# Performance work log

Hardware: AMD Instinct MI355X
Metric: run time of the kernel (lower is better)

## Reference

```python
import jax, jax.numpy as jnp
import numpy as np

D = 1024  # in_features
H = 16    # head_num

def setup_inputs() -> dict:
    key = jax.random.key(0)
    ks = jax.random.split(key, 11)
    S, B = 2048, 2
    scale = 1.0 / np.sqrt(D)
    inp = {
        'q': jax.random.normal(ks[0], (S, B, D), jnp.float32),
        'k': jax.random.normal(ks[1], (S, B, D), jnp.float32),
        'v': jax.random.normal(ks[2], (S, B, D), jnp.float32),
        'Wq': jax.random.normal(ks[3], (D, D), jnp.float32) * scale,
        'Wk': jax.random.normal(ks[4], (D, D), jnp.float32) * scale,
        'Wv': jax.random.normal(ks[5], (D, D), jnp.float32) * scale,
        'Wo': jax.random.normal(ks[6], (D, D), jnp.float32) * scale,
        'bq': jax.random.normal(ks[7], (D,), jnp.float32) * 0.01,
        'bk': jax.random.normal(ks[8], (D,), jnp.float32) * 0.01,
        'bv': jax.random.normal(ks[9], (D,), jnp.float32) * 0.01,
        'bo': jax.random.normal(ks[10], (D,), jnp.float32) * 0.01,
    }
    return inp

def reference(q, k, v, Wq, Wk, Wv, Wo, bq, bk, bv, bo):
    # q,k,v: (S, B, D) -> (B, S, D)
    q = jnp.transpose(q, (1, 0, 2))
    k = jnp.transpose(k, (1, 0, 2))
    v = jnp.transpose(v, (1, 0, 2))
    # linear + ReLU (torch Linear: x @ W.T + b)
    qh = jax.nn.relu(q @ Wq.T + bq)
    kh = jax.nn.relu(k @ Wk.T + bk)
    vh = jax.nn.relu(v @ Wv.T + bv)
    B, S, _ = qh.shape
    hd = D // H
    # (B, S, H, hd) -> (B, H, S, hd)
    qh = qh.reshape(B, S, H, hd).transpose(0, 2, 1, 3)
    kh = kh.reshape(B, S, H, hd).transpose(0, 2, 1, 3)
    vh = vh.reshape(B, S, H, hd).transpose(0, 2, 1, 3)
    scores = jnp.einsum('bhsd,bhtd->bhst', qh, kh) / np.sqrt(hd).astype(np.float32)
    attn = jax.nn.softmax(scores, axis=-1)
    y = jnp.einsum('bhst,bhtd->bhsd', attn, vh)  # (B, H, S, hd)
    y = y.transpose(0, 2, 1, 3).reshape(B, S, D)
    y = jax.nn.relu(y @ Wo.T + bo)
    return jnp.transpose(y, (1, 0, 2))  # (S, B, D)
```

## Files before the change

### kernel.cpp

```cpp
#include <hip/hip_runtime.h>
#include <stdint.h>

typedef __attribute__((ext_vector_type(8))) short bf8v;
typedef __attribute__((ext_vector_type(4))) float f4v;
typedef __attribute__((ext_vector_type(16))) float f16v;
typedef __attribute__((ext_vector_type(4))) unsigned int u4v;

__device__ __forceinline__ unsigned short f2bf(float f) {
  unsigned int u = __float_as_uint(f);
  u += 0x7fffu + ((u >> 16) & 1u);
  return (unsigned short)(u >> 16);
}

__device__ __forceinline__ unsigned short f2h(float f) {
  _Float16 h = (_Float16)f;
  return __builtin_bit_cast(unsigned short, h);
}

__device__ __forceinline__ float h2f(unsigned short s) {
  return (float)__builtin_bit_cast(_Float16, s);
}

__device__ __forceinline__ void gload16(const void* g, void* l) {
  __builtin_amdgcn_global_load_lds(
      (__attribute__((address_space(1))) void*)reinterpret_cast<uintptr_t>(g),
      (__attribute__((address_space(3))) void*)reinterpret_cast<uintptr_t>(l),
      16, 0, 0);
}

__device__ __forceinline__ unsigned cvtpk(float lo, float hi) {
  unsigned r;
  asm("v_cvt_pk_bf16_f32 %0, %1, %2" : "=v"(r) : "v"(lo), "v"(hi));
  return r;
}

#define PAIR_SWAP(x, y) asm("v_permlane32_swap_b32 %0, %1" : "+v"(x), "+v"(y))

__global__ __launch_bounds__(256) void cvt_w(
    const float* __restrict__ s0, const float* __restrict__ s1,
    const float* __restrict__ s2, const float* __restrict__ s3,
    unsigned short* __restrict__ dst) {
  const size_t NW = (size_t)1 << 20;
  size_t i = ((size_t)blockIdx.x * 256 + threadIdx.x) * 8;
  int a = (int)(i >> 20);
  const float* src = (a == 0) ? s0 : (a == 1) ? s1 : (a == 2) ? s2 : s3;
  size_t off = i & (NW - 1);
  const f4v* sp = (const f4v*)(src + off);
  f4v x = sp[0], y = sp[1];
  bf8v r;
  r[0] = (short)f2bf(x[0]); r[1] = (short)f2bf(x[1]);
  r[2] = (short)f2bf(x[2]); r[3] = (short)f2bf(x[3]);
  r[4] = (short)f2bf(y[0]); r[5] = (short)f2bf(y[1]);
  r[6] = (short)f2bf(y[2]); r[7] = (short)f2bf(y[3]);
  *(bf8v*)(dst + i) = r;
}

template <int OMODE>
__device__ __forceinline__ void gemmA32r_body(
    unsigned short* Al, unsigned short* Bl,
    const float* __restrict__ A, const unsigned short* __restrict__ W,
    const float* __restrict__ bias, unsigned short* __restrict__ out) {
  const int tid = threadIdx.x;
  const int w = tid >> 6, l = tid & 63;
  const int lr = l >> 4, lc = l & 15;
  const int m0 = blockIdx.x * 128, n0 = blockIdx.y * 128;
  const int wr = w >> 1, wc = w & 1;

  f4v acc[4][4];
#pragma unroll
  for (int i = 0; i < 4; i++)
#pragma unroll
    for (int j = 0; j < 4; j++) acc[i][j] = (f4v)(0.0f);

  int eA[2], rA[2], kA[2];
#pragma unroll
  for (int i = 0; i < 2; i++) {
    int chunk = w * 2 + i;
    eA[i] = chunk * 512 + l * 8;
    rA[i] = eA[i] >> 5;
    kA[i] = eA[i] & 31;
  }

  const int NK = 32;
  f4v ar[2][2];

  auto A_LOAD = [&](int kk) {
#pragma unroll
    for (int i = 0; i < 2; i++) {
      const float* s = A + (size_t)(m0 + rA[i]) * 1024 + kk * 32 + kA[i];
      ar[i][0] = *(const f4v*)s;
      ar[i][1] = *(const f4v*)(s + 4);
    }
  };
  auto A_WRITE = [&](int buf) {
#pragma unroll
    for (int i = 0; i < 2; i++) {
      u4v aw;
      aw[0] = cvtpk(ar[i][0][0], ar[i][0][1]);
      aw[1] = cvtpk(ar[i][0][2], ar[i][0][3]);
      aw[2] = cvtpk(ar[i][1][0], ar[i][1][1]);
      aw[3] = cvtpk(ar[i][1][2], ar[i][1][3]);
      *(bf8v*)(Al + buf * 4096 + eA[i]) = __builtin_bit_cast(bf8v, aw);
    }
  };
  auto B_STAGE = [&](int buf, int kk) {
#pragma unroll
    for (int i = 0; i < 2; i++) {
      int chunk = w * 2 + i;
      int e = chunk * 512 + l * 8;
      int r = e >> 5, k = e & 31;
      gload16(W + (size_t)(n0 + r) * 1024 + kk * 32 + k, Bl + buf * 4096 + chunk * 512);
    }
  };

  A_LOAD(0);
  B_STAGE(0, 0);
  A_WRITE(0);
  __syncthreads();

  for (int kk = 0; kk < NK; kk++) {
    const int cur = kk & 1;
    const bool more = (kk + 1 < NK);
    if (more) {
      A_LOAD(kk + 1);
      B_STAGE(cur ^ 1, kk + 1);
    }
    bf8v av[4], bv[4];
#pragma unroll
    for (int i = 0; i < 4; i++) {
      int row = wr * 64 + i * 16 + lc;
      av[i] = *(const bf8v*)(Al + cur * 4096 + row * 32 + lr * 8);
    }
#pragma unroll
    for (int j = 0; j < 4; j++) {
      int row = wc * 64 + j * 16 + lc;
      bv[j] = *(const bf8v*)(Bl + cur * 4096 + row * 32 + lr * 8);
    }
#pragma unroll
    for (int i = 0; i < 4; i++)
#pragma unroll
      for (int j = 0; j < 4; j++)
        acc[i][j] = __builtin_amdgcn_mfma_f32_16x16x32_bf16(av[i], bv[j], acc[i][j], 0, 0, 0);
    if (more) A_WRITE(cur ^ 1);
    __syncthreads();
  }

#pragma unroll
  for (int j = 0; j < 4; j++) {
    int n = n0 + wc * 64 + j * 16 + lc;
    float bj = bias[n];
#pragma unroll
    for (int i = 0; i < 4; i++) {
      int mb = m0 + wr * 64 + i * 16 + lr * 4;
#pragma unroll
      for (int q = 0; q < 4; q++) {
        float val = fmaxf(acc[i][j][q] + bj, 0.0f);
        int m = mb + q;
        int s = m >> 1, b = m & 1;
        int h = n >> 6, d = n & 63;
        if (OMODE == 0)
          out[((size_t)(b * 16 + h) * 2048 + s) * 64 + d] = f2bf(val);
        else
          out[((size_t)(b * 16 + h) * 64 + d) * 2048 + s] = f2bf(val);
      }
    }
  }
}

__global__ __launch_bounds__(256) void qkv_gemm(
    const float* __restrict__ qA, const float* __restrict__ kA,
    const float* __restrict__ vA,
    const unsigned short* __restrict__ Wq, const unsigned short* __restrict__ Wk,
    const unsigned short* __restrict__ Wv,
    const float* __restrict__ bq, const float* __restrict__ bk,
    const float* __restrict__ bv,
    unsigned short* __restrict__ Qh, unsigned short* __restrict__ Kh,
    unsigned short* __restrict__ Vt) {
  __shared__ __align__(16) unsigned short Al[2 * 4096];
  __shared__ __align__(16) unsigned short Bl[2 * 4096];
  int z = blockIdx.z;
  if (z == 0)      gemmA32r_body<0>(Al, Bl, qA, Wq, bq, Qh);
  else if (z == 1) gemmA32r_body<0>(Al, Bl, kA, Wk, bk, Kh);
  else             gemmA32r_body<1>(Al, Bl, vA, Wv, bv, Vt);
}

template <int TN>
__device__ __forceinline__ void gemm_body2(
    unsigned short* Al, unsigned short* Bl,
    const unsigned short* __restrict__ A, const unsigned short* __restrict__ W,
    const float* __restrict__ bias, float* __restrict__ out) {
  const int tid = threadIdx.x;
  const int w = tid >> 6, l = tid & 63;
  const int lr = l >> 4, lc = l & 15;
  const int m0 = blockIdx.x * 128, n0 = blockIdx.y * TN;
  const int wr = w >> 1, wc = w & 1;
  const int JW = TN / 32;
  const int BCPW = TN / 64;
  const int BBUF = TN * 32;

  f4v acc[4][JW];
#pragma unroll
  for (int i = 0; i < 4; i++)
#pragma unroll
    for (int j = 0; j < JW; j++) acc[i][j] = (f4v)(0.0f);

  const int NK = 32;
#pragma unroll
  for (int i = 0; i < 2; i++) {
    int chunk = w * 2 + i;
    int e = chunk * 512 + l * 8;
    int r = e >> 5, k = e & 31;
    gload16(A + (size_t)(m0 + r) * 1024 + k, Al + chunk * 512);
  }
#pragma unroll
  for (int i = 0; i < BCPW; i++) {
    int chunk = w * BCPW + i;
    int e = chunk * 512 + l * 8;
    int r = e >> 5, k = e & 31;
    gload16(W + (size_t)(n0 + r) * 1024 + k, Bl + chunk * 512);
  }

  for (int kk = 0; kk < NK; kk++) {
    const int cur = kk & 1;
    __syncthreads();
    if (kk + 1 < NK) {
#pragma unroll
      for (int i = 0; i < 2; i++) {
        int chunk = w * 2 + i;
        int e = chunk * 512 + l * 8;
        int r = e >> 5, k = (kk + 1) * 32 + (e & 31);
        gload16(A + (size_t)(m0 + r) * 1024 + k, Al + (cur ^ 1) * 4096 + chunk * 512);
      }
#pragma unroll
      for (int i = 0; i < BCPW; i++) {
        int chunk = w * BCPW + i;
        int e = chunk * 512 + l * 8;
        int r = e >> 5, k = (kk + 1) * 32 + (e & 31);
        gload16(W + (size_t)(n0 + r) * 1024 + k, Bl + (cur ^ 1) * BBUF + chunk * 512);
      }
    }
    bf8v av[4], bv[JW];
#pragma unroll
    for (int i = 0; i < 4; i++) {
      int row = wr * 64 + i * 16 + lc;
      av[i] = *(const bf8v*)(Al + cur * 4096 + row * 32 + lr * 8);
    }
#pragma unroll
    for (int j = 0; j < JW; j++) {
      int row = wc * (TN / 2) + j * 16 + lc;
      bv[j] = *(const bf8v*)(Bl + cur * BBUF + row * 32 + lr * 8);
    }
#pragma unroll
    for (int i = 0; i < 4; i++)
#pragma unroll
      for (int j = 0; j < JW; j++)
        acc[i][j] = __builtin_amdgcn_mfma_f32_16x16x32_bf16(av[i], bv[j], acc[i][j], 0, 0, 0);
  }

#pragma unroll
  for (int j = 0; j < JW; j++) {
    int n = n0 + wc * (TN / 2) + j * 16 + lc;
    float bj = bias[n];
#pragma unroll
    for (int i = 0; i < 4; i++) {
      int mb = m0 + wr * 64 + i * 16 + lr * 4;
#pragma unroll
      for (int q = 0; q < 4; q++) {
        float val = fmaxf(acc[i][j][q] + bj, 0.0f);
        int m = mb + q;
        int s = m & 2047, b = m >> 11;
        out[(size_t)(s * 2 + b) * 1024 + n] = val;
      }
    }
  }
}

__global__ __launch_bounds__(256) void out_gemm(
    const unsigned short* __restrict__ Y, const unsigned short* __restrict__ Wo,
    const float* __restrict__ bo, float* __restrict__ out) {
  __shared__ __align__(16) unsigned short Al[2 * 4096];
  __shared__ __align__(16) unsigned short Bl[2 * 2048];
  gemm_body2<64>(Al, Bl, Y, Wo, bo, out);
}

__global__ __launch_bounds__(256, 2) void attn_kernel(
    const unsigned short* __restrict__ Qh, const unsigned short* __restrict__ Kh,
    const unsigned short* __restrict__ Vt,
    unsigned short* __restrict__ PO, float2* __restrict__ ML, int kvlen) {
  __shared__ __align__(16) unsigned short Kl[2][4096];
  __shared__ __align__(16) unsigned short Vl[2][4096];
  const int tid = threadIdx.x, w = tid >> 6, l = tid & 63;
  const int lo = l & 31, hi = l >> 5;
  const int bh = blockIdx.y;
  const int z = blockIdx.z;
  const int tbeg = z * kvlen, tend = tbeg + kvlen;
  const int q0 = blockIdx.x * 256 + w * 64;
  const size_t qkbase = (size_t)bh * 2048 * 64;
  const size_t vtbase = (size_t)bh * 64 * 2048;
  const float cs = 0.125f * 1.44269504088896341f;

  bf8v qf[2][4];
#pragma unroll
  for (int s = 0; s < 2; s++)
#pragma unroll
    for (int c = 0; c < 4; c++)
      qf[s][c] = *(const bf8v*)(Qh + qkbase + (size_t)(q0 + s * 32 + lo) * 64 + c * 16 + hi * 8);

  f16v oacc[2][2];
  oacc[0][0] = (f16v)(0.0f); oacc[0][1] = (f16v)(0.0f);
  oacc[1][0] = (f16v)(0.0f); oacc[1][1] = (f16v)(0.0f);
  float mrun[2] = {-1e30f, -1e30f};
  float lrun[2] = {0.0f, 0.0f};

  const int swl = (lo & 7) << 4;
  int akb[4], avb[2][2][2];
#pragma unroll
  for (int c = 0; c < 4; c++) akb[c] = lo * 128 + ((c * 32 + hi * 16) ^ swl);
#pragma unroll
  for (int dt = 0; dt < 2; dt++)
#pragma unroll
    for (int kvh = 0; kvh < 2; kvh++)
#pragma unroll
      for (int kc = 0; kc < 2; kc++)
        avb[dt][kvh][kc] = (dt * 32 + lo) * 128 + ((kvh * 64 + kc * 32 + hi * 16) ^ swl);

  int stE[2], stD[2], stKV[2];
#pragma unroll
  for (int i = 0; i < 2; i++) {
    int o = (w * 2 + i) * 1024 + l * 16;
    int row = o >> 7;
    stE[i] = (o ^ ((row & 7) << 4)) >> 1;
    stD[i] = stE[i] >> 6;
    stKV[i] = stE[i] & 63;
  }
  const char* KlB = (const char*)&Kl[0][0];
  const char* VlB = (const char*)&Vl[0][0];

  auto STAGE = [&](int buf, int t0) {
#pragma unroll
    for (int i = 0; i < 2; i++) {
      gload16(Kh + qkbase + (size_t)t0 * 64 + stE[i], (char*)&Kl[buf][0] + (w * 2 + i) * 1024);
      gload16(Vt + vtbase + (size_t)stD[i] * 2048 + t0 + stKV[i], (char*)&Vl[buf][0] + (w * 2 + i) * 1024);
    }
  };

  auto COMPUTE = [&](int bo) {
#pragma unroll
    for (int kvh = 0; kvh < 2; kvh++) {
      bf8v kf[4];
#pragma unroll
      for (int c = 0; c < 4; c++)
        kf[c] = *(const bf8v*)(KlB + bo + kvh * 4096 + akb[c]);
      f16v sa = (f16v)(0.0f), sb = (f16v)(0.0f);
      __builtin_amdgcn_s_setprio(1);
#pragma unroll
      for (int c = 0; c < 4; c++) {
        sa = __builtin_amdgcn_mfma_f32_32x32x16_bf16(kf[c], qf[0][c], sa, 0, 0, 0);
        sb = __builtin_amdgcn_mfma_f32_32x32x16_bf16(kf[c], qf[1][c], sb, 0, 0, 0);
      }
      __builtin_amdgcn_s_setprio(0);
      bf8v vf[2][2];
#pragma unroll
      for (int dt = 0; dt < 2; dt++)
#pragma unroll
        for (int kc = 0; kc < 2; kc++)
          vf[dt][kc] = *(const bf8v*)(VlB + bo + avb[dt][kvh][kc]);

#pragma unroll
      for (int s = 0; s < 2; s++) {
        const f16v& sc16 = (s == 0) ? sa : sb;
        float t0 = fmaxf(fmaxf(sc16[0], sc16[1]), sc16[2]);
        float t1 = fmaxf(fmaxf(sc16[3], sc16[4]), sc16[5]);
        float t2 = fmaxf(fmaxf(sc16[6], sc16[7]), sc16[8]);
        float t3 = fmaxf(fmaxf(sc16[9], sc16[10]), sc16[11]);
        float t4 = fmaxf(fmaxf(sc16[12], sc16[13]), sc16[14]);
        float lm = fmaxf(fmaxf(fmaxf(t0, t1), fmaxf(t2, t3)), fmaxf(t4, sc16[15]));
        float msc = lm * cs;
        if (!__all(msc <= mrun[s] + 5.0f)) {
          float x = msc, y = msc;
          PAIR_SWAP(x, y);
          float pm = fmaxf(x, y);
          float mnew = fmaxf(mrun[s], pm);
          float scl = __builtin_amdgcn_exp2f(mrun[s] - mnew);
          lrun[s] *= scl;
#pragma unroll
          for (int dt = 0; dt < 2; dt++)
#pragma unroll
            for (int r = 0; r < 16; r++) oacc[s][dt][r] *= scl;
          mrun[s] = mnew;
        }
        float p[16];
#pragma unroll
        for (int r = 0; r < 16; r++)
          p[r] = __builtin_amdgcn_exp2f(sc16[r] * cs - mrun[s]);
        float s01 = (p[0] + p[1]) + (p[2] + p[3]);
        float s23 = (p[4] + p[5]) + (p[6] + p[7]);
        float s45 = (p[8] + p[9]) + (p[10] + p[11]);
        float s67 = (p[12] + p[13]) + (p[14] + p[15]);
        lrun[s] += (s01 + s23) + (s45 + s67);
        bf8v pf[2];
#pragma unroll
        for (int kc = 0; kc < 2; kc++) {
          unsigned a0 = cvtpk(p[kc * 8 + 0], p[kc * 8 + 1]);
          unsigned a1 = cvtpk(p[kc * 8 + 2], p[kc * 8 + 3]);
          unsigned b0 = cvtpk(p[kc * 8 + 4], p[kc * 8 + 5]);
          unsigned b1 = cvtpk(p[kc * 8 + 6], p[kc * 8 + 7]);
          PAIR_SWAP(a0, b0);
          PAIR_SWAP(a1, b1);
          u4v pw;
          pw[0] = a0; pw[1] = a1; pw[2] = b0; pw[3] = b1;
          pf[kc] = __builtin_bit_cast(bf8v, pw);
        }
        __builtin_amdgcn_s_setprio(1);
#pragma unroll
        for (int dt = 0; dt < 2; dt++)
#pragma unroll
          for (int kc = 0; kc < 2; kc++)
            oacc[s][dt] = __builtin_amdgcn_mfma_f32_32x32x16_bf16(vf[dt][kc], pf[kc],
                                                                 oacc[s][dt], 0, 0, 0);
        __builtin_amdgcn_s_setprio(0);
      }
    }
  };

  STAGE(0, tbeg);
  __syncthreads();
#pragma unroll 1
  for (int t0 = tbeg; t0 < tend; t0 += 128) {
    STAGE(1, t0 + 64);
    COMPUTE(0);
    __syncthreads();
    if (t0 + 128 < tend) STAGE(0, t0 + 128);
    COMPUTE(8192);
    __syncthreads();
  }

#pragma unroll
  for (int s = 0; s < 2; s++) {
    float x = lrun[s], y = lrun[s];
    PAIR_SWAP(x, y);
    float lt = x + y;
    float inv = 1.0f / lt;
    int q = q0 + s * 32 + lo;
    size_t prow = (size_t)(z * 32 + bh) * 2048 + q;
    if (hi == 0) ML[prow] = float2{mrun[s], lt};
    unsigned short* pp = PO + prow * 64;
#pragma unroll
    for (int dt = 0; dt < 2; dt++)
#pragma unroll
      for (int r = 0; r < 16; r++) {
        int d = dt * 32 + (r & 3) + 8 * (r >> 2) + 4 * hi;
        pp[d] = f2h(oacc[s][dt][r] * inv);
      }
  }
}

__global__ __launch_bounds__(256) void combine_kernel(
    const unsigned short* __restrict__ PO, const float2* __restrict__ ML,
    unsigned short* __restrict__ Y) {
  int idx = blockIdx.x * 256 + threadIdx.x;
  int row = idx >> 1, hr = idx & 1;
  int bh = row >> 11, q = row & 2047;
  float2 ml0 = ML[row], ml1 = ML[65536 + row];
  float M = fmaxf(ml0.x, ml1.x);
  float w0 = ml0.y * __builtin_amdgcn_exp2f(ml0.x - M);
  float w1 = ml1.y * __builtin_amdgcn_exp2f(ml1.x - M);
  float invW = 1.0f / (w0 + w1);
  w0 *= invW; w1 *= invW;
  int b = bh >> 4, h = bh & 15;
  unsigned short* yp = Y + (((size_t)(b * 2048 + q)) << 10) + h * 64 + hr * 32;
  const unsigned short* p0 = PO + (size_t)row * 64 + hr * 32;
  const unsigned short* p1 = PO + ((size_t)65536 + row) * 64 + hr * 32;
#pragma unroll
  for (int g = 0; g < 4; g++) {
    bf8v v0 = *(const bf8v*)(p0 + g * 8);
    bf8v v1 = *(const bf8v*)(p1 + g * 8);
    bf8v r;
#pragma unroll
    for (int j = 0; j < 8; j++)
      r[j] = (short)f2bf(h2f((unsigned short)v0[j]) * w0 +
                         h2f((unsigned short)v1[j]) * w1);
    *(bf8v*)(yp + g * 8) = r;
  }
}

extern "C" void kernel_launch(void* const* d_in, const int* in_sizes, int n_in,
                              void* d_out, int out_size, void* d_ws, size_t ws_size,
                              hipStream_t stream) {
  const float* q  = (const float*)d_in[0];
  const float* k  = (const float*)d_in[1];
  const float* v  = (const float*)d_in[2];
  const float* Wq = (const float*)d_in[3];
  const float* Wk = (const float*)d_in[4];
  const float* Wv = (const float*)d_in[5];
  const float* Wo = (const float*)d_in[6];
  const float* bq = (const float*)d_in[7];
  const float* bk = (const float*)d_in[8];
  const float* bv = (const float*)d_in[9];
  const float* bo = (const float*)d_in[10];

  const size_t NA = (size_t)4096 * 1024;
  const size_t NW = (size_t)1024 * 1024;
  unsigned short* WqB = (unsigned short*)d_ws;
  unsigned short* WkB = WqB + NW;
  unsigned short* WvB = WkB + NW;
  unsigned short* WoB = WvB + NW;
  unsigned short* Qh  = WoB + NW;
  unsigned short* Kh  = Qh  + NA;
  unsigned short* Vt  = Kh  + NA;
  unsigned short* Y   = Vt  + NA;
  unsigned short* PO  = Y   + NA;
  float2*         ML  = (float2*)(PO + 2 * NA);

  cvt_w<<<dim3(2048), 256, 0, stream>>>(Wq, Wk, Wv, Wo, WqB);

  qkv_gemm<<<dim3(32, 8, 3), 256, 0, stream>>>(q, k, v, WqB, WkB, WvB,
                                               bq, bk, bv, Qh, Kh, Vt);
  attn_kernel<<<dim3(8, 32, 2), 256, 0, stream>>>(Qh, Kh, Vt, PO, ML, 1024);
  combine_kernel<<<dim3(512), 256, 0, stream>>>(PO, ML, Y);
  out_gemm<<<dim3(32, 16), 256, 0, stream>>>(Y, WoB, bo, (float*)d_out);
}
```

Baseline: 123.3 us.

## Deepen QKV GEMM register prefetch and double attention KV tile size

The projection GEMM now keeps two register sets of A data in flight, issuing global loads two k-steps ahead and unrolling the main loop by two. The attention kernel stages 128 KV positions per buffer instead of 64, with a wider 16-row XOR swizzle for the V tile. Both changes aim to hide global-memory latency and halve the number of barriers per KV token. The cost is more registers in the GEMM and double the LDS in attention (64 KB), which may limit occupancy under the launch bound of 2 blocks per CU.

```diff
diff --git a/kernel.cpp b/kernel.cpp
--- a/kernel.cpp
+++ b/kernel.cpp
@@ -81,10 +81,9 @@
     kA[i] = eA[i] & 31;
   }
 
-  const int NK = 32;
-  f4v ar[2][2];
-
-  auto A_LOAD = [&](int kk) {
+  f4v arA[2][2], arB[2][2];
+
+  auto A_LOAD = [&](f4v (&ar)[2][2], int kk) {
 #pragma unroll
     for (int i = 0; i < 2; i++) {
       const float* s = A + (size_t)(m0 + rA[i]) * 1024 + kk * 32 + kA[i];
@@ -92,7 +91,7 @@
       ar[i][1] = *(const f4v*)(s + 4);
     }
   };
-  auto A_WRITE = [&](int buf) {
+  auto A_WRITE = [&](f4v (&ar)[2][2], int buf) {
 #pragma unroll
     for (int i = 0; i < 2; i++) {
       u4v aw;
@@ -112,36 +111,42 @@
       gload16(W + (size_t)(n0 + r) * 1024 + kk * 32 + k, Bl + buf * 4096 + chunk * 512);
     }
   };
-
-  A_LOAD(0);
-  B_STAGE(0, 0);
-  A_WRITE(0);
-  __syncthreads();
-
-  for (int kk = 0; kk < NK; kk++) {
-    const int cur = kk & 1;
-    const bool more = (kk + 1 < NK);
-    if (more) {
-      A_LOAD(kk + 1);
-      B_STAGE(cur ^ 1, kk + 1);
-    }
+  auto FRAG_MFMA = [&](int buf) {
     bf8v av[4], bv[4];
 #pragma unroll
     for (int i = 0; i < 4; i++) {
       int row = wr * 64 + i * 16 + lc;
-      av[i] = *(const bf8v*)(Al + cur * 4096 + row * 32 + lr * 8);
+      av[i] = *(const bf8v*)(Al + buf * 4096 + row * 32 + lr * 8);
     }
 #pragma unroll
     for (int j = 0; j < 4; j++) {
       int row = wc * 64 + j * 16 + lc;
-      bv[j] = *(const bf8v*)(Bl + cur * 4096 + row * 32 + lr * 8);
+      bv[j] = *(const bf8v*)(Bl + buf * 4096 + row * 32 + lr * 8);
     }
 #pragma unroll
     for (int i = 0; i < 4; i++)
 #pragma unroll
       for (int j = 0; j < 4; j++)
         acc[i][j] = __builtin_amdgcn_mfma_f32_16x16x32_bf16(av[i], bv[j], acc[i][j], 0, 0, 0);
-    if (more) A_WRITE(cur ^ 1);
+  };
+
+  A_LOAD(arA, 0);
+  A_LOAD(arB, 1);
+  B_STAGE(0, 0);
+  A_WRITE(arA, 0);
+  __syncthreads();
+
+#pragma unroll 1
+  for (int kk = 0; kk < 32; kk += 2) {
+    if (kk + 2 < 32) A_LOAD(arA, kk + 2);
+    B_STAGE(1, kk + 1);
+    FRAG_MFMA(0);
+    A_WRITE(arB, 1);
+    __syncthreads();
+    if (kk + 3 < 32) A_LOAD(arB, kk + 3);
+    if (kk + 2 < 32) B_STAGE(0, kk + 2);
+    FRAG_MFMA(1);
+    if (kk + 2 < 32) A_WRITE(arA, 0);
     __syncthreads();
   }
 
@@ -287,8 +292,8 @@
     const unsigned short* __restrict__ Qh, const unsigned short* __restrict__ Kh,
     const unsigned short* __restrict__ Vt,
     unsigned short* __restrict__ PO, float2* __restrict__ ML, int kvlen) {
-  __shared__ __align__(16) unsigned short Kl[2][4096];
-  __shared__ __align__(16) unsigned short Vl[2][4096];
+  __shared__ __align__(16) unsigned short Kl[2][8192];
+  __shared__ __align__(16) unsigned short Vl[2][8192];
   const int tid = threadIdx.x, w = tid >> 6, l = tid & 63;
   const int lo = l & 31, hi = l >> 5;
   const int bh = blockIdx.y;
@@ -312,41 +317,44 @@
   float mrun[2] = {-1e30f, -1e30f};
   float lrun[2] = {0.0f, 0.0f};
 
-  const int swl = (lo & 7) << 4;
-  int akb[4], avb[2][2][2];
-#pragma unroll
-  for (int c = 0; c < 4; c++) akb[c] = lo * 128 + ((c * 32 + hi * 16) ^ swl);
+  const int swk = (lo & 7) << 4;
+  const int swv = (lo & 15) << 4;
+  int akb[4], avb[2][4][2];
+#pragma unroll
+  for (int c = 0; c < 4; c++) akb[c] = lo * 128 + ((c * 32 + hi * 16) ^ swk);
 #pragma unroll
   for (int dt = 0; dt < 2; dt++)
 #pragma unroll
-    for (int kvh = 0; kvh < 2; kvh++)
+    for (int kvh = 0; kvh < 4; kvh++)
 #pragma unroll
       for (int kc = 0; kc < 2; kc++)
-        avb[dt][kvh][kc] = (dt * 32 + lo) * 128 + ((kvh * 64 + kc * 32 + hi * 16) ^ swl);
-
-  int stE[2], stD[2], stKV[2];
-#pragma unroll
-  for (int i = 0; i < 2; i++) {
-    int o = (w * 2 + i) * 1024 + l * 16;
-    int row = o >> 7;
-    stE[i] = (o ^ ((row & 7) << 4)) >> 1;
-    stD[i] = stE[i] >> 6;
-    stKV[i] = stE[i] & 63;
+        avb[dt][kvh][kc] = (dt * 32 + lo) * 256 + ((kvh * 64 + kc * 32 + hi * 16) ^ swv);
+
+  int stKE[4], stVD[4], stVKV[4];
+#pragma unroll
+  for (int i = 0; i < 4; i++) {
+    int o = (w * 4 + i) * 1024 + l * 16;
+    int rK = o >> 7;
+    stKE[i] = (o ^ ((rK & 7) << 4)) >> 1;
+    int rV = o >> 8;
+    int eV = (o ^ ((rV & 15) << 4)) >> 1;
+    stVD[i] = eV >> 7;
+    stVKV[i] = eV & 127;
   }
   const char* KlB = (const char*)&Kl[0][0];
   const char* VlB = (const char*)&Vl[0][0];
 
   auto STAGE = [&](int buf, int t0) {
 #pragma unroll
-    for (int i = 0; i < 2; i++) {
-      gload16(Kh + qkbase + (size_t)t0 * 64 + stE[i], (char*)&Kl[buf][0] + (w * 2 + i) * 1024);
-      gload16(Vt + vtbase + (size_t)stD[i] * 2048 + t0 + stKV[i], (char*)&Vl[buf][0] + (w * 2 + i) * 1024);
+    for (int i = 0; i < 4; i++) {
+      gload16(Kh + qkbase + (size_t)t0 * 64 + stKE[i], (char*)&Kl[buf][0] + (w * 4 + i) * 1024);
+      gload16(Vt + vtbase + (size_t)stVD[i] * 2048 + t0 + stVKV[i], (char*)&Vl[buf][0] + (w * 4 + i) * 1024);
     }
   };
 
   auto COMPUTE = [&](int bo) {
 #pragma unroll
-    for (int kvh = 0; kvh < 2; kvh++) {
+    for (int kvh = 0; kvh < 4; kvh++) {
       bf8v kf[4];
 #pragma unroll
       for (int c = 0; c < 4; c++)
@@ -426,12 +434,12 @@
   STAGE(0, tbeg);
   __syncthreads();
 #pragma unroll 1
-  for (int t0 = tbeg; t0 < tend; t0 += 128) {
-    STAGE(1, t0 + 64);
+  for (int t0 = tbeg; t0 < tend; t0 += 256) {
+    STAGE(1, t0 + 128);
     COMPUTE(0);
     __syncthreads();
-    if (t0 + 128 < tend) STAGE(0, t0 + 128);
-    COMPUTE(8192);
+    if (t0 + 256 < tend) STAGE(0, t0 + 256);
+    COMPUTE(16384);
     __syncthreads();
   }
 
```

After: 130.4 us. +5.8%, slower.
